# Optimization experiments

Hardware: AMD Instinct MI355X
Metric: run time of the kernel (lower is better)

## Reference

```python
import jax, jax.numpy as jnp
import numpy as np

HIDDEN = 1000
DICT = 4811
T = 44
B = 256


def _lstm_cell(x, h, c, W_ih, W_hh, b_ih, b_hh):
    # gates: [B, 4*H], PyTorch order i, f, g, o
    gates = x @ W_ih.T + b_ih + h @ W_hh.T + b_hh
    i, f, g, o = jnp.split(gates, 4, axis=-1)
    i = jax.nn.sigmoid(i)
    f = jax.nn.sigmoid(f)
    g = jnp.tanh(g)
    o = jax.nn.sigmoid(o)
    c_new = f * c + i * g
    h_new = o * jnp.tanh(c_new)
    return h_new, c_new


def setup_inputs() -> dict:
    key = jax.random.key(0)
    ks = jax.random.split(key, 20)
    s = 0.02
    H = HIDDEN
    return {
        "x": jax.random.normal(ks[0], (B, T, H), jnp.float32),
        "h1": jax.random.normal(ks[1], (B, H), jnp.float32),
        "h2": jax.random.normal(ks[2], (B, H), jnp.float32),
        "c1": jax.random.normal(ks[3], (B, H), jnp.float32),
        "c2": jax.random.normal(ks[4], (B, H), jnp.float32),
        "layer_W": jax.random.normal(ks[5], (H, H), jnp.float32) * s,
        "layer_b": jnp.zeros((H,), jnp.float32),
        "W_ih1": jax.random.normal(ks[6], (4 * H, 2 * H), jnp.float32) * s,
        "W_hh1": jax.random.normal(ks[7], (4 * H, H), jnp.float32) * s,
        "b_ih1": jnp.zeros((4 * H,), jnp.float32),
        "b_hh1": jnp.zeros((4 * H,), jnp.float32),
        "W_ih2": jax.random.normal(ks[8], (4 * H, DICT + 2 * H), jnp.float32) * s,
        "W_hh2": jax.random.normal(ks[9], (4 * H, H), jnp.float32) * s,
        "b_ih2": jnp.zeros((4 * H,), jnp.float32),
        "b_hh2": jnp.zeros((4 * H,), jnp.float32),
        "out_W": jax.random.normal(ks[10], (DICT, H), jnp.float32) * s,
        "out_b": jnp.zeros((DICT,), jnp.float32),
    }


def reference(x, h1, h2, c1, c2, layer_W, layer_b,
              W_ih1, W_hh1, b_ih1, b_hh1,
              W_ih2, W_hh2, b_ih2, b_hh2,
              out_W, out_b):
    # input projection: [B, T, H]
    xp = x @ layer_W.T + layer_b
    prev0 = jnp.zeros((x.shape[0], DICT), x.dtype)

    def step(carry, xt):
        h1, c1, h2, c2, prev = carry
        l1_in = jnp.concatenate([xt, h1], axis=1)            # [B, 2H]
        h1n, c1n = _lstm_cell(l1_in, h1, c1, W_ih1, W_hh1, b_ih1, b_hh1)
        l2_in = jnp.concatenate([prev, h2, h1n], axis=1)     # [B, DICT+2H]
        h2n, c2n = _lstm_cell(l2_in, h2, c2, W_ih2, W_hh2, b_ih2, b_hh2)
        logits = h2n @ out_W.T + out_b                       # [B, DICT]
        # NOTE: original torch code softmaxes over dim=0 (batch axis)
        y = jax.nn.softmax(logits, axis=0)
        return (h1n, c1n, h2n, c2n, y), y

    xs = jnp.transpose(xp, (1, 0, 2))                        # [T, B, H]
    _, ys = jax.lax.scan(step, (h1, c1, h2, c2, prev0), xs)
    return jnp.transpose(ys, (1, 0, 2))                      # [B, T, DICT]
```

## Files before the change

kernel.cpp:

```cpp
#include <hip/hip_runtime.h>
#include <hip/hip_bf16.h>

#define HID   1000
#define DICT  4811
#define TT    44
#define BB    256
#define G4    4000
#define G4P   4096
#define K1P   2048
#define K2P   6912
#define HP    1024
#define DP    4864
#define Z2_H2 4864
#define Z2_H1 5888
#define PD    3

typedef __attribute__((ext_vector_type(8))) short short8;
typedef __attribute__((ext_vector_type(4))) float f32x4;

__device__ __forceinline__ short f2b(float f) {
    unsigned u = __float_as_uint(f);
    unsigned r = (u + 0x7FFFu + ((u >> 16) & 1u)) >> 16;
    return (short)r;
}

__device__ __forceinline__ void gload16(const void* g, const short* l) {
    __builtin_amdgcn_global_load_lds(
        (const __attribute__((address_space(1))) unsigned int*)g,
        (__attribute__((address_space(3))) unsigned int*)l, 16, 0, 0);
}

__global__ void prep_w1p(const float* __restrict__ wih1, const float* __restrict__ whh1,
                         short* __restrict__ w) {
    for (size_t i = (size_t)blockIdx.x * blockDim.x + threadIdx.x; i < (size_t)G4P * K1P;
         i += (size_t)gridDim.x * blockDim.x) {
        int n = (int)(i >> 11), j = (int)(i & 2047);
        float v = 0.f;
        if (n < G4) {
            if (j < HID) v = wih1[(size_t)n * 2000 + j];
            else if (j >= 1024 && j < 1024 + HID) {
                int jj = j - 1024;
                v = wih1[(size_t)n * 2000 + HID + jj] + whh1[(size_t)n * HID + jj];
            }
        }
        w[i] = f2b(v);
    }
}

__global__ void prep_w2p(const float* __restrict__ wih2, const float* __restrict__ whh2,
                         short* __restrict__ w) {
    int n = blockIdx.y;
    int j = blockIdx.x * 256 + threadIdx.x;
    float v = 0.f;
    if (n < G4) {
        if (j < DICT) v = wih2[(size_t)n * 6811 + j];
        else if (j >= Z2_H2 && j < Z2_H2 + HID) {
            int jj = j - Z2_H2;
            v = wih2[(size_t)n * 6811 + DICT + jj] + whh2[(size_t)n * HID + jj];
        } else if (j >= Z2_H1 && j < Z2_H1 + HID) {
            int jj = j - Z2_H1;
            v = wih2[(size_t)n * 6811 + DICT + HID + jj];
        }
    }
    w[(size_t)n * K2P + j] = f2b(v);
}

__global__ void prep_outwp(const float* __restrict__ outw, short* __restrict__ w) {
    int n = blockIdx.y;
    int j = blockIdx.x * 256 + threadIdx.x;
    float v = (n < DICT && j < HID) ? outw[(size_t)n * HID + j] : 0.f;
    w[(size_t)n * HP + j] = f2b(v);
}

__global__ void prep_cvt(const float* __restrict__ src, short* __restrict__ dst, size_t n) {
    for (size_t i = (size_t)blockIdx.x * blockDim.x + threadIdx.x; i < n;
         i += (size_t)gridDim.x * blockDim.x)
        dst[i] = f2b(src[i]);
}

__global__ void prep_addv(const float* __restrict__ a, const float* __restrict__ b,
                          float* __restrict__ dst, int n) {
    int i = blockIdx.x * blockDim.x + threadIdx.x;
    if (i < n) dst[i] = a[i] + b[i];
}

__global__ void init_vec(const float* __restrict__ src, short* __restrict__ dst, int ld) {
    int i = blockIdx.x * blockDim.x + threadIdx.x;
    if (i >= BB * HID) return;
    int b = i / HID, h = i % HID;
    dst[(size_t)b * ld + h] = f2b(src[i]);
}

template <int EPI, int AF32>
__global__ __launch_bounds__(256) void gemm_nt(
    const void* __restrict__ Ap, int lda,
    const short* __restrict__ Bp, int ldb,
    const float* __restrict__ bias,
    void* __restrict__ Cp, long long partStride, int ldc,
    int M, int N, int Kvalid)
{
    __shared__ short As[64][40];
    __shared__ short Bs[64][40];
    const int tid  = threadIdx.x;
    const int lane = tid & 63;
    const int wave = tid >> 6;
    const int wm = wave >> 1, wn = wave & 1;
    const int tm = blockIdx.y * 64, tn = blockIdx.x * 64;
    const int srow = tid >> 2;
    const int scol = (tid & 3) * 8;

    const int nk = (Kvalid + 31) >> 5;
    const int s0 = (int)(((long long)nk * blockIdx.z) / gridDim.z);
    const int s1 = (int)(((long long)nk * (blockIdx.z + 1)) / gridDim.z);

    const int arow = tm + srow;
    const int brow = tn + srow;
    const bool bvalid = brow < N;

    auto loadA = [&](int ks) -> short8 {
        int k = (ks << 5) + scol;
        short8 r = {0, 0, 0, 0, 0, 0, 0, 0};
        if (k + 8 <= Kvalid) {
            if (AF32) {
                const f32x4* p = (const f32x4*)((const float*)Ap + (size_t)arow * lda + k);
                f32x4 u0 = p[0], u1 = p[1];
                r[0] = f2b(u0[0]); r[1] = f2b(u0[1]); r[2] = f2b(u0[2]); r[3] = f2b(u0[3]);
                r[4] = f2b(u1[0]); r[5] = f2b(u1[1]); r[6] = f2b(u1[2]); r[7] = f2b(u1[3]);
            } else {
                r = *(const short8*)((const short*)Ap + (size_t)arow * lda + k);
            }
        }
        return r;
    };
    auto loadB = [&](int ks) -> short8 {
        int k = (ks << 5) + scol;
        short8 r = {0, 0, 0, 0, 0, 0, 0, 0};
        if (bvalid && (k + 8 <= Kvalid))
            r = *(const short8*)(Bp + (size_t)brow * ldb + k);
        return r;
    };

    f32x4 acc[2][2];
    for (int a = 0; a < 2; ++a)
        for (int b = 0; b < 2; ++b)
            acc[a][b] = (f32x4){0.f, 0.f, 0.f, 0.f};

    short8 ra = loadA(s0), rb = loadB(s0);
    *(short8*)&As[srow][scol] = ra;
    *(short8*)&Bs[srow][scol] = rb;
    __syncthreads();

    const int kg = (lane >> 4) * 8;
    const int fr = lane & 15;

    for (int s = s0; s < s1; ++s) {
        short8 a0 = *(short8*)&As[wm * 32 + fr][kg];
        short8 a1 = *(short8*)&As[wm * 32 + 16 + fr][kg];
        short8 b0 = *(short8*)&Bs[wn * 32 + fr][kg];
        short8 b1 = *(short8*)&Bs[wn * 32 + 16 + fr][kg];
        short8 na, nb;
        if (s + 1 < s1) { na = loadA(s + 1); nb = loadB(s + 1); }
        acc[0][0] = __builtin_amdgcn_mfma_f32_16x16x32_bf16(a0, b0, acc[0][0], 0, 0, 0);
        acc[0][1] = __builtin_amdgcn_mfma_f32_16x16x32_bf16(a0, b1, acc[0][1], 0, 0, 0);
        acc[1][0] = __builtin_amdgcn_mfma_f32_16x16x32_bf16(a1, b0, acc[1][0], 0, 0, 0);
        acc[1][1] = __builtin_amdgcn_mfma_f32_16x16x32_bf16(a1, b1, acc[1][1], 0, 0, 0);
        __syncthreads();
        if (s + 1 < s1) {
            *(short8*)&As[srow][scol] = na;
            *(short8*)&Bs[srow][scol] = nb;
        }
        __syncthreads();
    }

    float* Cf = (float*)Cp + (size_t)partStride * blockIdx.z;
    for (int mi = 0; mi < 2; ++mi)
        for (int ni = 0; ni < 2; ++ni) {
            int col = tn + wn * 32 + ni * 16 + (lane & 15);
            if (col >= N) continue;
            float bv = bias ? bias[col] : 0.f;
            int row0 = tm + wm * 32 + mi * 16 + ((lane >> 4) << 2);
            f32x4 v = acc[mi][ni];
            for (int j = 0; j < 4; ++j) {
                int row = row0 + j;
                float val = v[j] + bv;
                if (EPI == 0) {
                    Cf[(size_t)row * ldc + col] = val;
                } else {
                    int b = row / TT, t = row % TT;
                    ((short*)Cp)[((size_t)t * BB + b) * ldc + col] = f2b(val);
                }
            }
        }
}

__global__ __launch_bounds__(512) void gemm_step3(
    const short* __restrict__ A0, const short* __restrict__ A1, int splitA, int lda,
    const short* __restrict__ Bw, int ldb,
    float* __restrict__ C, long long partStride, int ldc, int nk)
{
    __shared__ __align__(16) short smem[PD][12288];
    const int tid  = threadIdx.x;
    const int lane = tid & 63;
    const int w    = tid >> 6;
    const int wm = w >> 1, wn = w & 1;
    const int tn = blockIdx.x * 128;
    const int s0 = (int)(((long long)nk * blockIdx.z) / gridDim.z);
    const int s1 = (int)(((long long)nk * (blockIdx.z + 1)) / gridDim.z);

    const int cA0 = w * 64 + lane;
    const int cA1 = cA0 + 512;
    const int rA0 = cA0 >> 2, rA1 = cA1 >> 2;
    const size_t aoff0 = (size_t)rA0 * lda + (size_t)((((cA0 & 3) ^ ((rA0 >> 1) & 3))) << 3);
    const size_t aoff1 = (size_t)rA1 * lda + (size_t)((((cA1 & 3) ^ ((rA1 >> 1) & 3))) << 3);
    const int cB = w * 64 + lane;
    const int rB = cB >> 2;
    const size_t boff = (size_t)(tn + rB) * ldb + (size_t)((((cB & 3) ^ ((rB >> 1) & 3))) << 3);

    auto stage = [&](int buf, int s) {
        const int k0 = s << 5;
        const short* As = (k0 < splitA) ? A0 : A1;
        const short* l = &smem[buf][0];
        gload16(As + k0 + aoff0, l + w * 512);
        gload16(As + k0 + aoff1, l + 4096 + w * 512);
        gload16(Bw + k0 + boff,  l + 8192 + w * 512);
    };

    const int fr = lane & 15;
    const int kg = lane >> 4;
    int aRd[4], bRd[4];
    #pragma unroll
    for (int mi = 0; mi < 4; ++mi) {
        int row = wm * 64 + mi * 16 + fr;
        aRd[mi] = row * 32 + ((kg ^ ((row >> 1) & 3)) << 3);
    }
    #pragma unroll
    for (int ni = 0; ni < 4; ++ni) {
        int row = wn * 64 + ni * 16 + fr;
        bRd[ni] = 8192 + row * 32 + ((kg ^ ((row >> 1) & 3)) << 3);
    }

    f32x4 acc[4][4];
    #pragma unroll
    for (int a = 0; a < 4; ++a)
        #pragma unroll
        for (int b = 0; b < 4; ++b)
            acc[a][b] = (f32x4){0.f, 0.f, 0.f, 0.f};

    #pragma unroll
    for (int i = 0; i < PD; ++i)
        if (s0 + i < s1) stage(i, s0 + i);

    int buf = 0;
    for (int s = s0; s < s1; ++s) {
        const int ahead = s1 - 1 - s;
        if (ahead >= 2)      asm volatile("s_waitcnt vmcnt(6)" ::: "memory");
        else if (ahead == 1) asm volatile("s_waitcnt vmcnt(3)" ::: "memory");
        else                 asm volatile("s_waitcnt vmcnt(0)" ::: "memory");
        __builtin_amdgcn_s_barrier();

        const short* bp = &smem[buf][0];
        short8 af[4], bf[4];
        #pragma unroll
        for (int i = 0; i < 4; ++i) af[i] = *(const short8*)(bp + aRd[i]);
        #pragma unroll
        for (int i = 0; i < 4; ++i) bf[i] = *(const short8*)(bp + bRd[i]);
        asm volatile("s_waitcnt lgkmcnt(0)" ::: "memory");
        __builtin_amdgcn_sched_barrier(0);
        __builtin_amdgcn_s_barrier();
        if (s + PD < s1) stage(buf, s + PD);

        #pragma unroll
        for (int mi = 0; mi < 4; ++mi)
            #pragma unroll
            for (int ni = 0; ni < 4; ++ni)
                acc[mi][ni] = __builtin_amdgcn_mfma_f32_16x16x32_bf16(af[mi], bf[ni], acc[mi][ni], 0, 0, 0);

        buf = (buf + 1 == PD) ? 0 : buf + 1;
    }

    float* Cp = C + (size_t)partStride * blockIdx.z;
    const int colb = tn + wn * 64 + fr;
    const int rowb = wm * 64 + (kg << 2);
    #pragma unroll
    for (int mi = 0; mi < 4; ++mi)
        #pragma unroll
        for (int ni = 0; ni < 4; ++ni) {
            int col = colb + ni * 16;
            int row0 = rowb + mi * 16;
            #pragma unroll
            for (int j = 0; j < 4; ++j)
                Cp[(size_t)(row0 + j) * ldc + col] = acc[mi][ni][j];
        }
}

template <int NP>
__global__ void lstm_ewN(const float* __restrict__ g, long long ps,
                         const float* __restrict__ bias, float* __restrict__ c,
                         short* __restrict__ d1, int ld1,
                         short* __restrict__ d2, int ld2)
{
    int i = blockIdx.x * blockDim.x + threadIdx.x;
    if (i >= BB * HID) return;
    int b = i / HID, h = i % HID;
    size_t base = (size_t)b * G4P + h;
    float gi = bias[h], gf = bias[HID + h], gg = bias[2 * HID + h], go = bias[3 * HID + h];
    #pragma unroll
    for (int p = 0; p < NP; ++p) {
        const float* gp = g + (size_t)ps * p + base;
        gi += gp[0];
        gf += gp[HID];
        gg += gp[2 * HID];
        go += gp[3 * HID];
    }
    float ii = 1.f / (1.f + expf(-gi));
    float ff = 1.f / (1.f + expf(-gf));
    float tg = tanhf(gg);
    float oo = 1.f / (1.f + expf(-go));
    float cn = ff * c[i] + ii * tg;
    c[i] = cn;
    float hn = oo * tanhf(cn);
    short hb = f2b(hn);
    d1[(size_t)b * ld1 + h] = hb;
    d2[(size_t)b * ld2 + h] = hb;
}

template <int NP>
__global__ __launch_bounds__(256) void softmaxN(
    const float* __restrict__ lg, long long ps, const float* __restrict__ outb,
    float* __restrict__ out, short* __restrict__ z2, int t)
{
    __shared__ float red[8][32];
    const int dl = threadIdx.x & 31;
    const int bg = threadIdx.x >> 5;
    const int d = blockIdx.x * 32 + dl;
    const bool valid = d < DICT;
    float v[32];
    float m = -1e30f;
    if (valid) {
        const float bv = outb[d];
        #pragma unroll
        for (int i = 0; i < 32; ++i) {
            size_t o = (size_t)(bg * 32 + i) * DP + d;
            float x = bv;
            #pragma unroll
            for (int p = 0; p < NP; ++p) x += lg[(size_t)ps * p + o];
            v[i] = x;
            m = fmaxf(m, x);
        }
    } else {
        #pragma unroll
        for (int i = 0; i < 32; ++i) v[i] = 0.f;
    }
    red[bg][dl] = m;
    __syncthreads();
    m = red[0][dl];
    #pragma unroll
    for (int r = 1; r < 8; ++r) m = fmaxf(m, red[r][dl]);
    float s = 0.f;
    #pragma unroll
    for (int i = 0; i < 32; ++i) { v[i] = expf(v[i] - m); s += v[i]; }
    __syncthreads();
    red[bg][dl] = s;
    __syncthreads();
    s = 0.f;
    #pragma unroll
    for (int r = 0; r < 8; ++r) s += red[r][dl];
    const float inv = 1.f / s;
    if (valid) {
        #pragma unroll
        for (int i = 0; i < 32; ++i) {
            int b = bg * 32 + i;
            float y = v[i] * inv;
            out[(size_t)b * ((size_t)TT * DICT) + (size_t)t * DICT + d] = y;
            z2[(size_t)b * K2P + d] = f2b(y);
        }
    }
}

extern "C" void kernel_launch(void* const* d_in, const int* in_sizes, int n_in,
                              void* d_out, int out_size, void* d_ws, size_t ws_size,
                              hipStream_t stream)
{
    const float* x    = (const float*)d_in[0];
    const float* h1   = (const float*)d_in[1];
    const float* h2   = (const float*)d_in[2];
    const float* c1in = (const float*)d_in[3];
    const float* c2in = (const float*)d_in[4];
    const float* layW = (const float*)d_in[5];
    const float* layb = (const float*)d_in[6];
    const float* Wih1 = (const float*)d_in[7];
    const float* Whh1 = (const float*)d_in[8];
    const float* bih1 = (const float*)d_in[9];
    const float* bhh1 = (const float*)d_in[10];
    const float* Wih2 = (const float*)d_in[11];
    const float* Whh2 = (const float*)d_in[12];
    const float* bih2 = (const float*)d_in[13];
    const float* bhh2 = (const float*)d_in[14];
    const float* outW = (const float*)d_in[15];
    const float* outb = (const float*)d_in[16];
    float* out = (float*)d_out;
    (void)in_sizes; (void)n_in; (void)out_size; (void)ws_size;

    char* ws = (char*)d_ws;
    size_t off = 0;
    auto alloc = [&](size_t bytes) -> void* {
        size_t p = off;
        off = (off + bytes + 255) & ~(size_t)255;
        return (void*)(ws + p);
    };

    short* w1cat = (short*)alloc((size_t)G4P * K1P * 2);
    short* w2cat = (short*)alloc((size_t)G4P * K2P * 2);
    short* outwb = (short*)alloc((size_t)DP * HP * 2);
    short* laywb = (short*)alloc((size_t)HID * HID * 2);
    short* xp    = (short*)alloc((size_t)TT * BB * HP * 2);
    short* h1pad = (short*)alloc((size_t)BB * HP * 2);
    short* h2pad = (short*)alloc((size_t)BB * HP * 2);
    short* z2    = (short*)alloc((size_t)BB * K2P * 2);
    float* gbuf  = (float*)alloc((size_t)8 * BB * G4P * 4);
    float* lgtp  = (float*)alloc((size_t)4 * BB * DP * 4);
    float* c1    = (float*)alloc((size_t)BB * HID * 4);
    float* c2    = (float*)alloc((size_t)BB * HID * 4);
    float* bias1 = (float*)alloc((size_t)G4 * 4);
    float* bias2 = (float*)alloc((size_t)G4 * 4);

    hipMemsetAsync(xp, 0, (size_t)TT * BB * HP * 2, stream);
    hipMemsetAsync(z2, 0, (size_t)BB * K2P * 2, stream);
    hipMemsetAsync(h1pad, 0, (size_t)BB * HP * 2, stream);
    hipMemsetAsync(h2pad, 0, (size_t)BB * HP * 2, stream);

    prep_w1p<<<4096, 256, 0, stream>>>(Wih1, Whh1, w1cat);
    prep_w2p<<<dim3(27, G4P), 256, 0, stream>>>(Wih2, Whh2, w2cat);
    prep_outwp<<<dim3(4, DP), 256, 0, stream>>>(outW, outwb);
    prep_cvt<<<1024, 256, 0, stream>>>(layW, laywb, (size_t)HID * HID);
    prep_addv<<<16, 256, 0, stream>>>(bih1, bhh1, bias1, G4);
    prep_addv<<<16, 256, 0, stream>>>(bih2, bhh2, bias2, G4);
    init_vec<<<1000, 256, 0, stream>>>(h1, h1pad, HP);
    init_vec<<<1000, 256, 0, stream>>>(h2, h2pad, HP);
    init_vec<<<1000, 256, 0, stream>>>(h2, z2 + Z2_H2, K2P);
    hipMemcpyAsync(c1, c1in, (size_t)BB * HID * 4, hipMemcpyDeviceToDevice, stream);
    hipMemcpyAsync(c2, c2in, (size_t)BB * HID * 4, hipMemcpyDeviceToDevice, stream);

    gemm_nt<1, 1><<<dim3(16, (BB * TT) / 64, 1), 256, 0, stream>>>(
        x, HID, laywb, HID, layb, xp, 0, HP, BB * TT, HID, HID);

    const long long GP = (long long)BB * G4P;
    const long long LP = (long long)BB * DP;

    for (int t = 0; t < TT; ++t) {
        gemm_step3<<<dim3(32, 1, 4), 512, 0, stream>>>(
            xp + (size_t)t * BB * HP, h1pad - HP, 1024, HP, w1cat, K1P, gbuf, GP, G4P, K1P / 32);
        lstm_ewN<4><<<1000, 256, 0, stream>>>(gbuf, GP, bias1, c1, z2 + Z2_H1, K2P, h1pad, HP);

        gemm_step3<<<dim3(32, 1, 8), 512, 0, stream>>>(
            z2, z2, 0, K2P, w2cat, K2P, gbuf, GP, G4P, K2P / 32);
        lstm_ewN<8><<<1000, 256, 0, stream>>>(gbuf, GP, bias2, c2, z2 + Z2_H2, K2P, h2pad, HP);

        gemm_step3<<<dim3(38, 1, 4), 512, 0, stream>>>(
            h2pad, h2pad, 0, HP, outwb, HP, lgtp, LP, DP, HP / 32);

        softmaxN<4><<<151, 256, 0, stream>>>(lgtp, LP, outb, out, z2, t);
    }
}
```

Baseline: 3.510 ms.

## Fuse output-projection GEMM with batch-axis softmax into one kernel

Replaces the split-K output logits GEMM plus the separate softmax kernel with a single kernel. Each block computes all 256 batch rows for 64 dictionary columns over the full K, then does the column-wise (batch axis) softmax in registers and shared memory before writing the output and the bf16 copy into z2. This removes the fp32 partial-logits round trip through global memory and one launch per timestep. In exchange it drops split-K, so only 76 blocks each run the full K loop, which lowers parallelism for that GEMM.

```diff
diff --git a/kernel.cpp b/kernel.cpp
--- a/kernel.cpp
+++ b/kernel.cpp
@@ -14,6 +14,7 @@
 #define Z2_H2 4864
 #define Z2_H1 5888
 #define PD    3
+#define GPART ((long long)BB * G4P)
 
 typedef __attribute__((ext_vector_type(8))) short short8;
 typedef __attribute__((ext_vector_type(4))) float f32x4;
@@ -293,6 +294,169 @@
         }
 }
 
+__global__ __launch_bounds__(512) void logits_sm(
+    const short* __restrict__ A , const short* __restrict__ Bw ,
+    const float* __restrict__ outb, float* __restrict__ out,
+    short* __restrict__ z2, int t)
+{
+    __shared__ __align__(16) short smem[PD][10240];
+    __shared__ float red[256];
+    const int tid  = threadIdx.x;
+    const int lane = tid & 63;
+    const int w    = tid >> 6;
+    const int wm = w >> 1, wn = w & 1;
+    const int tn = blockIdx.x * 64;
+    const int nk = HP / 32;
+
+    const int cA0 = w * 64 + lane;
+    const int cA1 = cA0 + 512;
+    const int rA0 = cA0 >> 2, rA1 = cA1 >> 2;
+    const size_t aoff0 = (size_t)rA0 * HP + (size_t)((((cA0 & 3) ^ ((rA0 >> 1) & 3))) << 3);
+    const size_t aoff1 = (size_t)rA1 * HP + (size_t)((((cA1 & 3) ^ ((rA1 >> 1) & 3))) << 3);
+    const int cB = w * 32 + (lane & 31);
+    const int rB = cB >> 2;
+    const size_t boff = (size_t)(tn + rB) * HP + (size_t)((((cB & 3) ^ ((rB >> 1) & 3))) << 3);
+
+    auto stage = [&](int buf, int s) {
+        const int k0 = s << 5;
+        const short* l = &smem[buf][0];
+        gload16(A + k0 + aoff0, l + w * 512);
+        gload16(A + k0 + aoff1, l + 4096 + w * 512);
+        if (lane < 32) gload16(Bw + k0 + boff, l + 8192 + w * 256);
+    };
+
+    const int fr = lane & 15;
+    const int kg = lane >> 4;
+    int aRd[4], bRd[2];
+    #pragma unroll
+    for (int mi = 0; mi < 4; ++mi) {
+        int row = wm * 64 + mi * 16 + fr;
+        aRd[mi] = row * 32 + ((kg ^ ((row >> 1) & 3)) << 3);
+    }
+    #pragma unroll
+    for (int ni = 0; ni < 2; ++ni) {
+        int row = wn * 32 + ni * 16 + fr;
+        bRd[ni] = 8192 + row * 32 + ((kg ^ ((row >> 1) & 3)) << 3);
+    }
+
+    f32x4 acc[4][2];
+    #pragma unroll
+    for (int a = 0; a < 4; ++a)
+        #pragma unroll
+        for (int b = 0; b < 2; ++b)
+            acc[a][b] = (f32x4){0.f, 0.f, 0.f, 0.f};
+
+    #pragma unroll
+    for (int i = 0; i < PD; ++i) stage(i, i);
+
+    int buf = 0;
+    for (int s = 0; s < nk; ++s) {
+        const int ahead = nk - 1 - s;
+        if (ahead >= 2)      asm volatile("s_waitcnt vmcnt(6)" ::: "memory");
+        else if (ahead == 1) asm volatile("s_waitcnt vmcnt(3)" ::: "memory");
+        else                 asm volatile("s_waitcnt vmcnt(0)" ::: "memory");
+        __builtin_amdgcn_s_barrier();
+
+        const short* bp = &smem[buf][0];
+        short8 af[4], bf[2];
+        #pragma unroll
+        for (int i = 0; i < 4; ++i) af[i] = *(const short8*)(bp + aRd[i]);
+        #pragma unroll
+        for (int i = 0; i < 2; ++i) bf[i] = *(const short8*)(bp + bRd[i]);
+        asm volatile("s_waitcnt lgkmcnt(0)" ::: "memory");
+        __builtin_amdgcn_sched_barrier(0);
+        __builtin_amdgcn_s_barrier();
+        if (s + PD < nk) stage(buf, s + PD);
+
+        #pragma unroll
+        for (int mi = 0; mi < 4; ++mi)
+            #pragma unroll
+            for (int ni = 0; ni < 2; ++ni)
+                acc[mi][ni] = __builtin_amdgcn_mfma_f32_16x16x32_bf16(af[mi], bf[ni], acc[mi][ni], 0, 0, 0);
+
+        buf = (buf + 1 == PD) ? 0 : buf + 1;
+    }
+
+    int   colv[2];
+    float bv[2];
+    #pragma unroll
+    for (int ni = 0; ni < 2; ++ni) {
+        colv[ni] = tn + wn * 32 + ni * 16 + fr;
+        bv[ni] = (colv[ni] < DICT) ? outb[colv[ni]] : 0.f;
+    }
+    float v[4][2][4];
+    float mx[2] = {-3e38f, -3e38f};
+    #pragma unroll
+    for (int mi = 0; mi < 4; ++mi)
+        #pragma unroll
+        for (int ni = 0; ni < 2; ++ni)
+            #pragma unroll
+            for (int j = 0; j < 4; ++j) {
+                float x = acc[mi][ni][j] + bv[ni];
+                v[mi][ni][j] = x;
+                mx[ni] = fmaxf(mx[ni], x);
+            }
+    #pragma unroll
+    for (int ni = 0; ni < 2; ++ni) {
+        mx[ni] = fmaxf(mx[ni], __shfl_xor(mx[ni], 16));
+        mx[ni] = fmaxf(mx[ni], __shfl_xor(mx[ni], 32));
+    }
+    if (lane < 16) {
+        red[wm * 64 + wn * 32 + fr]      = mx[0];
+        red[wm * 64 + wn * 32 + 16 + fr] = mx[1];
+    }
+    __syncthreads();
+    float m[2];
+    #pragma unroll
+    for (int ni = 0; ni < 2; ++ni) {
+        int c = wn * 32 + ni * 16 + fr;
+        m[ni] = fmaxf(fmaxf(red[c], red[64 + c]), fmaxf(red[128 + c], red[192 + c]));
+    }
+    __syncthreads();
+    float s2[2] = {0.f, 0.f};
+    #pragma unroll
+    for (int mi = 0; mi < 4; ++mi)
+        #pragma unroll
+        for (int ni = 0; ni < 2; ++ni)
+            #pragma unroll
+            for (int j = 0; j < 4; ++j) {
+                float e = expf(v[mi][ni][j] - m[ni]);
+                v[mi][ni][j] = e;
+                s2[ni] += e;
+            }
+    #pragma unroll
+    for (int ni = 0; ni < 2; ++ni) {
+        s2[ni] += __shfl_xor(s2[ni], 16);
+        s2[ni] += __shfl_xor(s2[ni], 32);
+    }
+    if (lane < 16) {
+        red[wm * 64 + wn * 32 + fr]      = s2[0];
+        red[wm * 64 + wn * 32 + 16 + fr] = s2[1];
+    }
+    __syncthreads();
+    float inv[2];
+    #pragma unroll
+    for (int ni = 0; ni < 2; ++ni) {
+        int c = wn * 32 + ni * 16 + fr;
+        inv[ni] = 1.f / (red[c] + red[64 + c] + red[128 + c] + red[192 + c]);
+    }
+    const int rowb = wm * 64 + (kg << 2);
+    #pragma unroll
+    for (int mi = 0; mi < 4; ++mi)
+        #pragma unroll
+        for (int j = 0; j < 4; ++j) {
+            int b = rowb + mi * 16 + j;
+            #pragma unroll
+            for (int ni = 0; ni < 2; ++ni) {
+                if (colv[ni] < DICT) {
+                    float y = v[mi][ni][j] * inv[ni];
+                    out[(size_t)b * ((size_t)TT * DICT) + (size_t)t * DICT + colv[ni]] = y;
+                    z2[(size_t)b * K2P + colv[ni]] = f2b(y);
+                }
+            }
+        }
+}
+
 template <int NP>
 __global__ void lstm_ewN(const float* __restrict__ g, long long ps,
                          const float* __restrict__ bias, float* __restrict__ c,
@@ -322,59 +486,6 @@
     short hb = f2b(hn);
     d1[(size_t)b * ld1 + h] = hb;
     d2[(size_t)b * ld2 + h] = hb;
-}
-
-template <int NP>
-__global__ __launch_bounds__(256) void softmaxN(
-    const float* __restrict__ lg, long long ps, const float* __restrict__ outb,
-    float* __restrict__ out, short* __restrict__ z2, int t)
-{
-    __shared__ float red[8][32];
-    const int dl = threadIdx.x & 31;
-    const int bg = threadIdx.x >> 5;
-    const int d = blockIdx.x * 32 + dl;
-    const bool valid = d < DICT;
-    float v[32];
-    float m = -1e30f;
-    if (valid) {
-        const float bv = outb[d];
-        #pragma unroll
-        for (int i = 0; i < 32; ++i) {
-            size_t o = (size_t)(bg * 32 + i) * DP + d;
-            float x = bv;
-            #pragma unroll
-            for (int p = 0; p < NP; ++p) x += lg[(size_t)ps * p + o];
-            v[i] = x;
-            m = fmaxf(m, x);
-        }
-    } else {
-        #pragma unroll
-        for (int i = 0; i < 32; ++i) v[i] = 0.f;
-    }
-    red[bg][dl] = m;
-    __syncthreads();
-    m = red[0][dl];
-    #pragma unroll
-    for (int r = 1; r < 8; ++r) m = fmaxf(m, red[r][dl]);
-    float s = 0.f;
-    #pragma unroll
-    for (int i = 0; i < 32; ++i) { v[i] = expf(v[i] - m); s += v[i]; }
-    __syncthreads();
-    red[bg][dl] = s;
-    __syncthreads();
-    s = 0.f;
-    #pragma unroll
-    for (int r = 0; r < 8; ++r) s += red[r][dl];
-    const float inv = 1.f / s;
-    if (valid) {
-        #pragma unroll
-        for (int i = 0; i < 32; ++i) {
-            int b = bg * 32 + i;
-            float y = v[i] * inv;
-            out[(size_t)b * ((size_t)TT * DICT) + (size_t)t * DICT + d] = y;
-            z2[(size_t)b * K2P + d] = f2b(y);
-        }
-    }
 }
 
 extern "C" void kernel_launch(void* const* d_in, const int* in_sizes, int n_in,
@@ -418,7 +529,6 @@
     short* h2pad = (short*)alloc((size_t)BB * HP * 2);
     short* z2    = (short*)alloc((size_t)BB * K2P * 2);
     float* gbuf  = (float*)alloc((size_t)8 * BB * G4P * 4);
-    float* lgtp  = (float*)alloc((size_t)4 * BB * DP * 4);
     float* c1    = (float*)alloc((size_t)BB * HID * 4);
     float* c2    = (float*)alloc((size_t)BB * HID * 4);
     float* bias1 = (float*)alloc((size_t)G4 * 4);
@@ -444,21 +554,15 @@
     gemm_nt<1, 1><<<dim3(16, (BB * TT) / 64, 1), 256, 0, stream>>>(
         x, HID, laywb, HID, layb, xp, 0, HP, BB * TT, HID, HID);
 
-    const long long GP = (long long)BB * G4P;
-    const long long LP = (long long)BB * DP;
-
     for (int t = 0; t < TT; ++t) {
         gemm_step3<<<dim3(32, 1, 4), 512, 0, stream>>>(
-            xp + (size_t)t * BB * HP, h1pad - HP, 1024, HP, w1cat, K1P, gbuf, GP, G4P, K1P / 32);
-        lstm_ewN<4><<<1000, 256, 0, stream>>>(gbuf, GP, bias1, c1, z2 + Z2_H1, K2P, h1pad, HP);
+            xp + (size_t)t * BB * HP, h1pad - HP, 1024, HP, w1cat, K1P, gbuf, GPART, G4P, K1P / 32);
+        lstm_ewN<4><<<1000, 256, 0, stream>>>(gbuf, GPART, bias1, c1, z2 + Z2_H1, K2P, h1pad, HP);
 
         gemm_step3<<<dim3(32, 1, 8), 512, 0, stream>>>(
-            z2, z2, 0, K2P, w2cat, K2P, gbuf, GP, G4P, K2P / 32);
-        lstm_ewN<8><<<1000, 256, 0, stream>>>(gbuf, GP, bias2, c2, z2 + Z2_H2, K2P, h2pad, HP);
-
-        gemm_step3<<<dim3(38, 1, 4), 512, 0, stream>>>(
-            h2pad, h2pad, 0, HP, outwb, HP, lgtp, LP, DP, HP / 32);
-
-        softmaxN<4><<<151, 256, 0, stream>>>(lgtp, LP, outb, out, z2, t);
-    }
-}
+            z2, z2, 0, K2P, w2cat, K2P, gbuf, GPART, G4P, K2P / 32);
+        lstm_ewN<8><<<1000, 256, 0, stream>>>(gbuf, GPART, bias2, c2, z2 + Z2_H2, K2P, h2pad, HP);
+
+        logits_sm<<<76, 512, 0, stream>>>(h2pad, outwb, outb, out, z2, t);
+    }
+}
```

Measured after the change: 3.587 ms. 2.2% more time.
